# Kernel optimization log

Hardware: AMD Instinct MI355X
Metric: run time of the kernel (lower is better)

## Reference

```python
import jax, jax.numpy as jnp
import numpy as np

CHUNK = 256
ROPE_BASE = 10000.0
EPS = 1e-6


def setup_inputs() -> dict:
    key = jax.random.key(0)
    ks = jax.random.split(key, 8)
    B, N, D, H, K = 4, 8192, 1024, 16, 4
    x = jax.random.normal(ks[0], (B, N, D), dtype=jnp.float32)
    norm_scale = jnp.ones((D,), dtype=jnp.float32)
    conv_w = jax.random.normal(ks[1], (D, 1, K), dtype=jnp.float32) * 0.2
    conv_b = jax.random.normal(ks[2], (D,), dtype=jnp.float32) * 0.02
    in_proj_w = jax.random.normal(ks[3], (D, 3 * D), dtype=jnp.float32) * 0.02
    dt_bias = jax.random.normal(ks[4], (D,), dtype=jnp.float32) * 0.5
    head_mix = jnp.eye(H, dtype=jnp.float32) + 0.02 * jax.random.normal(ks[5], (H, H), dtype=jnp.float32)
    out_proj_w = jax.random.normal(ks[6], (D, D), dtype=jnp.float32) * 0.02
    return {"x": x, "norm_scale": norm_scale, "conv_w": conv_w, "conv_b": conv_b,
            "in_proj_w": in_proj_w, "dt_bias": dt_bias, "head_mix": head_mix,
            "out_proj_w": out_proj_w}


def _rmsnorm(x, scale):
    xf = x.astype(jnp.float32)
    rms = jax.lax.rsqrt(jnp.mean(xf * xf, axis=-1, keepdims=True) + EPS)
    out = scale.astype(jnp.float32) * (xf * rms)
    return jnp.clip(out, -60000.0, 60000.0).astype(x.dtype)


def _rope(v, N, d_head, dtype):
    # v: (B, N, H, d_head); cos/sin: (N, d_head//2)
    half = d_head // 2
    inv_freq = 1.0 / (ROPE_BASE ** (jnp.arange(0, d_head, 2, dtype=jnp.float32) / d_head))
    freqs = jnp.arange(N, dtype=jnp.float32)[:, None] * inv_freq[None, :]
    cos = jnp.cos(freqs).astype(dtype)[None, :, None, :]
    sin = jnp.sin(freqs).astype(dtype)[None, :, None, :]
    v1, v2 = v[..., :half], v[..., half:]
    return jnp.concatenate([v1 * cos - v2 * sin, v1 * sin + v2 * cos], axis=-1)


def reference(x, norm_scale, conv_w, conv_b, in_proj_w, dt_bias, head_mix, out_proj_w):
    residual = x
    B, N, D = x.shape
    H = head_mix.shape[0]
    d_head = D // H
    xn = _rmsnorm(x, norm_scale)

    # depthwise causal conv: torch pads K-1 both sides then truncates to N -> left-pad only
    K = conv_w.shape[-1]
    xc = jax.lax.conv_general_dilated(
        xn.transpose(0, 2, 1), conv_w, window_strides=(1,), padding=[(K - 1, 0)],
        feature_group_count=D, dimension_numbers=("NCH", "OIH", "NCH"))
    xc = (xc + conv_b[None, :, None]).transpose(0, 2, 1)  # (B, N, D)
    xc = xc * jax.nn.sigmoid(xc)  # SiLU

    fused = xc @ in_proj_w  # (B, N, 3D)
    dt_raw, v, gate_raw = jnp.split(fused, 3, axis=-1)
    dt = jnp.clip(jax.nn.softplus(dt_raw.astype(jnp.float32) + dt_bias.astype(jnp.float32)),
                  0.001, 2.0).astype(dt_raw.dtype)
    gate = jax.nn.sigmoid(gate_raw)
    log_alpha = -dt.astype(jnp.float32)

    v_rot = _rope(v.reshape(B, N, H, d_head), N, d_head, x.dtype).reshape(B, N, D)
    v_in = (v_rot * dt).astype(jnp.float32)

    # pad to multiple of CHUNK (static)
    pad = (-N) % CHUNK
    if pad:
        v_in = jnp.pad(v_in, ((0, 0), (0, pad), (0, 0)))
        log_alpha = jnp.pad(log_alpha, ((0, 0), (0, pad), (0, 0)))
    Np = N + pad
    nc = Np // CHUNK
    v_ch = v_in.reshape(B, nc, CHUNK, D)
    la_ch = log_alpha.reshape(B, nc, CHUNK, D)

    # intra-chunk stabilized cumulative scan
    L = jnp.clip(jnp.cumsum(la_ch, axis=2), -20.0, 0.0)
    L_max = jnp.max(L, axis=2, keepdims=True)
    L_st = L - L_max
    cum_scaled = jnp.cumsum(jnp.exp(-L_st) * v_ch, axis=2)
    chunk_out = jnp.exp(L_st) * cum_scaled  # (B, nc, CHUNK, D)

    if nc > 1:
        # inter-chunk carry, fully parallel
        bdecay = L[:, :, -1, :]            # (B, nc, D)
        bout = chunk_out[:, :, -1, :]      # (B, nc, D)
        cum_decay = jnp.clip(jnp.cumsum(bdecay, axis=1), -80.0, 0.0)
        stab = jnp.max(cum_decay, axis=1, keepdims=True)
        ncd = jnp.clip(cum_decay - stab, -20.0, 0.0)
        seeds = bout * jnp.exp(-ncd)
        shifted = jnp.pad(seeds[:, :-1], ((0, 0), (1, 0), (0, 0)))
        carries = jnp.cumsum(shifted, axis=1) * jnp.exp(ncd)  # (B, nc, D)
        final = chunk_out + carries[:, :, None, :] * jnp.exp(L)
    else:
        final = chunk_out
    final = final.astype(x.dtype).reshape(B, Np, D)[:, :N, :]

    v_mix = jnp.einsum("bnhd,hm->bnmd", final.reshape(B, N, H, d_head), head_mix)
    final = v_mix.reshape(B, N, D)
    out = (final * gate) @ out_proj_w
    return residual + out
```

## Files before the change

### kernel.cpp

```cpp
#include <hip/hip_runtime.h>

#define TOK 32768
#define DMODEL 1024
#define NSEQ 8192
#define NCHK 32
#define CHUNKC 256
#define KDIM 1024
#define NKT (KDIM / 32)
#define LOG2E 1.44269504f

typedef __attribute__((ext_vector_type(8))) short bf16x8;
typedef __attribute__((ext_vector_type(4))) float f32x4;

__device__ __forceinline__ unsigned short f2bf(float f) {
  unsigned u = __float_as_uint(f);
  u += 0x7fffu + ((u >> 16) & 1u);
  return (unsigned short)(u >> 16);
}
__device__ __forceinline__ float bf2f(unsigned short h) {
  return __uint_as_float(((unsigned)h) << 16);
}
__device__ __forceinline__ float sigm(float x) {
  return __builtin_amdgcn_rcpf(1.f + exp2f(-LOG2E * x));
}

typedef __attribute__((address_space(3))) unsigned int lds_u32_t;
typedef const __attribute__((address_space(1))) unsigned int glb_u32_t;

__device__ __forceinline__ void gl_lds16(const void* g, void* l) {
  __builtin_amdgcn_global_load_lds((glb_u32_t*)g, (lds_u32_t*)l, 16, 0, 0);
}

__global__ __launch_bounds__(256) void transpose_bf16_k(const float* __restrict__ in,
                                                        unsigned short* __restrict__ out,
                                                        int R, int C) {
  __shared__ float tile[32][33];
  const int c0 = blockIdx.x * 32, r0 = blockIdx.y * 32;
  const int tx = threadIdx.x, ty = threadIdx.y;
#pragma unroll
  for (int i = 0; i < 32; i += 8)
    tile[ty + i][tx] = in[(long)(r0 + ty + i) * C + c0 + tx];
  __syncthreads();
#pragma unroll
  for (int i = 0; i < 32; i += 8)
    out[(long)(c0 + ty + i) * R + r0 + tx] = f2bf(tile[tx][ty + i]);
}

__global__ __launch_bounds__(256) void ropetab_k(float2* __restrict__ tab) {
  const int i = blockIdx.x * 256 + threadIdx.x;
  const int f = i & 31, n = i >> 5;
  const float invf = exp2f(-(float)f * (13.287712379549449f / 32.0f));
  const float ang = (float)n * invf;
  tab[i] = make_float2(cosf(ang), sinf(ang));
}

__global__ __launch_bounds__(256) void rmsconv_k(const float* __restrict__ x,
                                                 const float* __restrict__ scale,
                                                 const float* __restrict__ w,
                                                 const float* __restrict__ cb,
                                                 unsigned short* __restrict__ xc) {
  __shared__ float xs[11][1024];
  __shared__ float red[4];
  const int t = threadIdx.x;
  const long row0 = (long)blockIdx.x * 8;
  const bool seqstart = ((row0 & (NSEQ - 1)) == 0);
  const float4 sc = ((const float4*)scale)[t];
  for (int i = 0; i < 11; ++i) {
    if (i < 3 && seqstart) {
      ((float4*)xs[i])[t] = make_float4(0.f, 0.f, 0.f, 0.f);
      continue;
    }
    const long r = row0 - 3 + i;
    const float4 v = ((const float4*)(x + r * DMODEL))[t];
    float ss = v.x * v.x + v.y * v.y + v.z * v.z + v.w * v.w;
#pragma unroll
    for (int off = 32; off > 0; off >>= 1) ss += __shfl_down(ss, off);
    if ((t & 63) == 0) red[t >> 6] = ss;
    __syncthreads();
    const float tot = red[0] + red[1] + red[2] + red[3];
    const float rr = rsqrtf(tot * (1.0f / DMODEL) + 1e-6f);
    float4 o;
    o.x = fminf(fmaxf(v.x * rr * sc.x, -60000.f), 60000.f);
    o.y = fminf(fmaxf(v.y * rr * sc.y, -60000.f), 60000.f);
    o.z = fminf(fmaxf(v.z * rr * sc.z, -60000.f), 60000.f);
    o.w = fminf(fmaxf(v.w * rr * sc.w, -60000.f), 60000.f);
    ((float4*)xs[i])[t] = o;
    __syncthreads();
  }
  __syncthreads();
  const int d0 = t * 4;
  float wl[4][4];
#pragma unroll
  for (int j = 0; j < 4; ++j) {
    const float4 t4 = *(const float4*)(w + (d0 + j) * 4);
    wl[j][0] = t4.x; wl[j][1] = t4.y; wl[j][2] = t4.z; wl[j][3] = t4.w;
  }
  const float4 cb4 = ((const float4*)cb)[t];
#pragma unroll
  for (int orow = 0; orow < 8; ++orow) {
    float o[4] = {0.f, 0.f, 0.f, 0.f};
#pragma unroll
    for (int k = 0; k < 4; ++k) {
      const float4 xv = ((const float4*)xs[orow + k])[t];
      o[0] += xv.x * wl[0][k]; o[1] += xv.y * wl[1][k];
      o[2] += xv.z * wl[2][k]; o[3] += xv.w * wl[3][k];
    }
    ushort4 st;
    { const float a = o[0] + cb4.x; st.x = f2bf(a * sigm(a)); }
    { const float a = o[1] + cb4.y; st.y = f2bf(a * sigm(a)); }
    { const float a = o[2] + cb4.z; st.z = f2bf(a * sigm(a)); }
    { const float a = o[3] + cb4.w; st.w = f2bf(a * sigm(a)); }
    *(ushort4*)(xc + (row0 + orow) * DMODEL + d0) = st;
  }
}

template <int EPI, int NBN, int SBN>
__global__ __launch_bounds__(256) void gemm_bt(const unsigned short* __restrict__ A,
                                               const unsigned short* __restrict__ BT,
                                               unsigned short* __restrict__ ob,
                                               float* __restrict__ of,
                                               const float* __restrict__ resid) {
  __shared__ unsigned short As[3][128 * 32];
  __shared__ unsigned short Bs[3][256 * 32];
  const int tid = threadIdx.x;
  const int l = tid & 63;
  const int w = tid >> 6;
  constexpr int NC = (EPI == 0) ? 3072 : 1024;

  constexpr int BPS = 4 * SBN;
  constexpr int NBNS = NBN / SBN;
  const int lin = blockIdx.y * NBN + blockIdx.x;
  const int xcd = lin & 7;
  const int g = lin >> 3;
  const int s = g / BPS;
  const int r = g - s * BPS;
  const int bmo = r / SBN;
  const int bno = r - bmo * SBN;
  const int bmS = s / NBNS;
  const int bnS = s - bmS * NBNS;
  const int bm = xcd * 32 + bmS * 4 + bmo;
  const int bn = bnS * SBN + bno;

  f32x4 acc[8][4];
#pragma unroll
  for (int m = 0; m < 8; ++m)
#pragma unroll
    for (int n = 0; n < 4; ++n) acc[m][n] = {0.f, 0.f, 0.f, 0.f};

  const int srcc = (((l & 3) ^ ((l >> 3) & 3)) * 8);
  const unsigned short* aG0 = A + ((long)(bm * 128 + w * 32 + (l >> 2))) * KDIM + srcc;
  const unsigned short* bG0 = BT + ((long)(bn * 256 + w * 64 + (l >> 2))) * KDIM + srcc;
  const int aLo = (w * 32) * 32;
  const int bLo = (w * 64) * 32;

#define STAGE(buf, k0)                                           \
  {                                                              \
    gl_lds16(aG0 + (k0),             &As[buf][aLo]);             \
    gl_lds16(aG0 + (k0) + 16 * KDIM, &As[buf][aLo + 512]);       \
    gl_lds16(bG0 + (k0),             &Bs[buf][bLo]);             \
    gl_lds16(bG0 + (k0) + 16 * KDIM, &Bs[buf][bLo + 512]);       \
    gl_lds16(bG0 + (k0) + 32 * KDIM, &Bs[buf][bLo + 1024]);      \
    gl_lds16(bG0 + (k0) + 48 * KDIM, &Bs[buf][bLo + 1536]);      \
  }

  const int eoff = (((l >> 4) ^ ((l >> 1) & 3)) * 8);
  const int arow0 = (l & 15) * 32 + eoff;
  const int brow0 = (w * 64 + (l & 15)) * 32 + eoff;

  auto compute = [&](int cur) {
    const unsigned short* Ab = &As[cur][0];
    const unsigned short* Bb = &Bs[cur][0];
    bf16x8 af[8], bfr[4];
#pragma unroll
    for (int m = 0; m < 8; ++m) af[m] = *(const bf16x8*)&Ab[arow0 + m * 512];
#pragma unroll
    for (int n = 0; n < 4; ++n) bfr[n] = *(const bf16x8*)&Bb[brow0 + n * 512];
    __builtin_amdgcn_s_setprio(1);
#pragma unroll
    for (int m = 0; m < 8; ++m)
#pragma unroll
      for (int n = 0; n < 4; ++n)
        acc[m][n] = __builtin_amdgcn_mfma_f32_16x16x32_bf16(af[m], bfr[n], acc[m][n], 0, 0, 0);
    __builtin_amdgcn_s_setprio(0);
  };

  STAGE(0, 0);
  STAGE(1, 32);
  asm volatile("s_waitcnt vmcnt(6)" ::: "memory");
  int cur = 0, nxt = 2;
  for (int t = 0; t < NKT - 2; ++t) {
    __builtin_amdgcn_s_barrier();
    __builtin_amdgcn_sched_barrier(0);
    STAGE(nxt, (t + 2) * 32);
    compute(cur);
    asm volatile("s_waitcnt vmcnt(6)" ::: "memory");
    cur = (cur == 2) ? 0 : cur + 1;
    nxt = (nxt == 2) ? 0 : nxt + 1;
  }
  __builtin_amdgcn_s_barrier();
  __builtin_amdgcn_sched_barrier(0);
  compute(cur);
  asm volatile("s_waitcnt vmcnt(0)" ::: "memory");
  cur = (cur == 2) ? 0 : cur + 1;
  __builtin_amdgcn_s_barrier();
  __builtin_amdgcn_sched_barrier(0);
  compute(cur);
#undef STAGE

  const int rbase = bm * 128;
  const int cbase = bn * 256 + w * 64;
  const int lr4 = (l >> 4) * 4;
  const int lc16 = l & 15;

  if constexpr (EPI == 0) {
#pragma unroll
    for (int m = 0; m < 8; ++m)
#pragma unroll
      for (int n = 0; n < 4; ++n) {
        const int col = cbase + n * 16 + lc16;
#pragma unroll
        for (int j2 = 0; j2 < 4; ++j2) {
          const int row = rbase + m * 16 + lr4 + j2;
          ob[(long)row * NC + col] = f2bf(acc[m][n][j2]);
        }
      }
  } else {
#pragma unroll
    for (int m = 0; m < 8; ++m)
#pragma unroll
      for (int n = 0; n < 4; ++n) {
        const int col = cbase + n * 16 + lc16;
#pragma unroll
        for (int j2 = 0; j2 < 4; ++j2) {
          const int row = rbase + m * 16 + lr4 + j2;
          const long o = (long)row * NC + col;
          of[o] = resid[o] + acc[m][n][j2];
        }
      }
  }
}

__global__ __launch_bounds__(256) void scan1_k(const unsigned short* __restrict__ fu,
                                               const float* __restrict__ dt_bias,
                                               const float2* __restrict__ tab,
                                               float* __restrict__ Llast,
                                               float* __restrict__ bout) {
  const int idx = blockIdx.x * 256 + threadIdx.x;
  const int d = idx & 1023;
  const int ch = (idx >> 10) & 31;
  const int b = idx >> 15;
  const long base = ((long)b * NSEQ + ch * CHUNKC) * 3072 + d;
  const float bias = dt_bias[d];
  const int f = d & 31;
  const bool hi = (d & 32) != 0;
  const int po = hi ? -32 : 32;
  float run = 0.f, s = 0.f, L = 0.f;
#pragma unroll 4
  for (int c = 0; c < CHUNKC; ++c) {
    const long o = base + (long)c * 3072;
    const float a = bf2f(fu[o]) + bias;
    const float e2 = exp2f(-LOG2E * fabsf(a));
    const float sp = fmaxf(a, 0.f) + 0.69314718f * log2f(1.f + e2);
    const float dtv = fminf(fmaxf(sp, 0.001f), 2.0f);
    const float own = bf2f(fu[o + 1024]);
    const float oth = bf2f(fu[o + 1024 + po]);
    const float2 cs = tab[(ch * CHUNKC + c) * 32 + f];
    const float vr = own * cs.x + (hi ? oth * cs.y : -oth * cs.y);
    run -= dtv;
    L = fminf(fmaxf(run, -20.f), 0.f);
    s += exp2f(-LOG2E * L) * (vr * dtv);
  }
  Llast[idx] = L;
  bout[idx] = exp2f(LOG2E * L) * s;
}

__global__ __launch_bounds__(256) void scan2_k(const float* __restrict__ Llast,
                                               const float* __restrict__ bout,
                                               float* __restrict__ carry) {
  const int idx = blockIdx.x * 256 + threadIdx.x;
  const int d = idx & 1023;
  const int b = idx >> 10;
  const long base = (long)b * (NCHK * DMODEL) + d;
  float cd[NCHK];
  float run = 0.f, stab = -1e30f;
#pragma unroll
  for (int ch = 0; ch < NCHK; ++ch) {
    run += Llast[base + ch * DMODEL];
    cd[ch] = fminf(fmaxf(run, -80.f), 0.f);
    stab = fmaxf(stab, cd[ch]);
  }
  float acc = 0.f;
#pragma unroll
  for (int ch = 0; ch < NCHK; ++ch) {
    const float ncd = fminf(fmaxf(cd[ch] - stab, -20.f), 0.f);
    carry[base + ch * DMODEL] = acc * exp2f(LOG2E * ncd);
    acc += bout[base + ch * DMODEL] * exp2f(-LOG2E * ncd);
  }
}

__global__ __launch_bounds__(256) void scan3_k(unsigned short* fu,
                                               const float* __restrict__ dt_bias,
                                               const float2* __restrict__ tab,
                                               const float* __restrict__ carry) {
  const int idx = blockIdx.x * 256 + threadIdx.x;
  const int d = idx & 1023;
  const int ch = (idx >> 10) & 31;
  const int b = idx >> 15;
  const long base = ((long)b * NSEQ + ch * CHUNKC) * 3072 + d;
  const float bias = dt_bias[d];
  const int f = d & 31;
  const bool hi = (d & 32) != 0;
  const int po = hi ? -32 : 32;
  const float ce = carry[idx];
  float run = 0.f, s = 0.f;
#pragma unroll 4
  for (int c = 0; c < CHUNKC; ++c) {
    const long o = base + (long)c * 3072;
    const float a = bf2f(fu[o]) + bias;
    const float e2 = exp2f(-LOG2E * fabsf(a));
    const float sp = fmaxf(a, 0.f) + 0.69314718f * log2f(1.f + e2);
    const float dtv = fminf(fmaxf(sp, 0.001f), 2.0f);
    const float own = bf2f(fu[o + 1024]);
    const float oth = bf2f(fu[o + 1024 + po]);
    const float2 cs = tab[(ch * CHUNKC + c) * 32 + f];
    const float vr = own * cs.x + (hi ? oth * cs.y : -oth * cs.y);
    run -= dtv;
    const float L = fminf(fmaxf(run, -20.f), 0.f);
    s += exp2f(-LOG2E * L) * (vr * dtv);
    fu[o + 1024] = f2bf(exp2f(LOG2E * L) * (s + ce));
  }
}

__global__ __launch_bounds__(256) void headmix_k(const unsigned short* __restrict__ fu,
                                                 const float* __restrict__ hm,
                                                 unsigned short* __restrict__ A2) {
  __shared__ float mixs[256];
  const int t = threadIdx.x;
  mixs[t] = hm[t];
  __syncthreads();
  const long row = (long)blockIdx.x * 4 + (t >> 6);
  const int dd = t & 63;
  const unsigned short* fv0 = fu + row * 3072 + 1024 + dd;
  const unsigned short* gv0 = fu + row * 3072 + 2048 + dd;
  float fv[16];
#pragma unroll
  for (int h = 0; h < 16; ++h) fv[h] = bf2f(fv0[h * 64]);
#pragma unroll
  for (int m = 0; m < 16; ++m) {
    float o = 0.f;
#pragma unroll
    for (int h = 0; h < 16; ++h) o += fv[h] * mixs[h * 16 + m];
    A2[row * DMODEL + m * 64 + dd] = f2bf(o * sigm(bf2f(gv0[m * 64])));
  }
}

extern "C" void kernel_launch(void* const* d_in, const int* in_sizes, int n_in,
                              void* d_out, int out_size, void* d_ws, size_t ws_size,
                              hipStream_t stream) {
  const float* x        = (const float*)d_in[0];
  const float* nscale   = (const float*)d_in[1];
  const float* conv_w   = (const float*)d_in[2];
  const float* conv_b   = (const float*)d_in[3];
  const float* in_proj  = (const float*)d_in[4];
  const float* dt_bias  = (const float*)d_in[5];
  const float* head_mix = (const float*)d_in[6];
  const float* out_proj = (const float*)d_in[7];
  float* out = (float*)d_out;

  char* p = (char*)d_ws;
  unsigned short* W1T = (unsigned short*)p; p += (size_t)3072 * 1024 * 2;
  unsigned short* W2T = (unsigned short*)p; p += (size_t)1024 * 1024 * 2;
  float2* tab  = (float2*)p; p += (size_t)NSEQ * 32 * sizeof(float2);
  float* Llast = (float*)p;  p += (size_t)131072 * 4;
  float* bout  = (float*)p;  p += (size_t)131072 * 4;
  float* carry = (float*)p;  p += (size_t)131072 * 4;
  unsigned short* fusedb = (unsigned short*)p; p += (size_t)TOK * 3072 * 2;
  unsigned short* xc     = (unsigned short*)p; p += (size_t)TOK * DMODEL * 2;

  transpose_bf16_k<<<dim3(96, 32), dim3(32, 8), 0, stream>>>(in_proj, W1T, 1024, 3072);
  transpose_bf16_k<<<dim3(32, 32), dim3(32, 8), 0, stream>>>(out_proj, W2T, 1024, 1024);
  ropetab_k<<<1024, 256, 0, stream>>>(tab);
  rmsconv_k<<<TOK / 8, 256, 0, stream>>>(x, nscale, conv_w, conv_b, xc);

  gemm_bt<0, 12, 6><<<dim3(12, 256), 256, 0, stream>>>(xc, W1T, fusedb, nullptr, nullptr);
  scan1_k<<<512, 256, 0, stream>>>(fusedb, dt_bias, tab, Llast, bout);
  scan2_k<<<16, 256, 0, stream>>>(Llast, bout, carry);
  scan3_k<<<512, 256, 0, stream>>>(fusedb, dt_bias, tab, carry);
  headmix_k<<<TOK / 4, 256, 0, stream>>>(fusedb, head_mix, xc );
  gemm_bt<1, 4, 4><<<dim3(4, 256), 256, 0, stream>>>(xc, W2T, nullptr, out, x);
}
```

Baseline: 626.8 us.

## Restructure bf16 GEMM to 256x256 tiles with 8 waves and phased pipelining

The GEMM kernel moves from 128x256 tiles on 4 waves to 256x256 tiles on 8 waves (512 threads), with each wave computing a 128x64 sub-tile. The K loop becomes a two-buffer, two-substep schedule with 64-wide K steps. Each step is split into half-phases that interleave LDS fragment reads, async global-to-LDS staging and MFMA bursts, separated by barriers and explicit waitcnts. The goal is more data reuse per block and better overlap of loads with MFMA work. The cost is more barriers, larger LDS use (64 KB) and fewer blocks on the grid.

New measurement: 656.0 us. 1.05x slower.

```diff
diff --git a/kernel.cpp b/kernel.cpp
--- a/kernel.cpp
+++ b/kernel.cpp
@@ -6,7 +6,6 @@
 #define NCHK 32
 #define CHUNKC 256
 #define KDIM 1024
-#define NKT (KDIM / 32)
 #define LOG2E 1.44269504f
 
 typedef __attribute__((ext_vector_type(8))) short bf16x8;
@@ -115,16 +114,17 @@
 }
 
 template <int EPI, int NBN, int SBN>
-__global__ __launch_bounds__(256) void gemm_bt(const unsigned short* __restrict__ A,
+__global__ __launch_bounds__(512) void gemm_bt(const unsigned short* __restrict__ A,
                                                const unsigned short* __restrict__ BT,
                                                unsigned short* __restrict__ ob,
                                                float* __restrict__ of,
                                                const float* __restrict__ resid) {
-  __shared__ unsigned short As[3][128 * 32];
-  __shared__ unsigned short Bs[3][256 * 32];
+  __shared__ unsigned short As[2][2][8192];
+  __shared__ unsigned short Bs[2][2][8192];
   const int tid = threadIdx.x;
   const int l = tid & 63;
   const int w = tid >> 6;
+  const int wr = w >> 2, wc = w & 3;
   constexpr int NC = (EPI == 0) ? 3072 : 1024;
 
   constexpr int BPS = 4 * SBN;
@@ -138,7 +138,7 @@
   const int bno = r - bmo * SBN;
   const int bmS = s / NBNS;
   const int bnS = s - bmS * NBNS;
-  const int bm = xcd * 32 + bmS * 4 + bmo;
+  const int bm = xcd * 16 + bmS * 4 + bmo;
   const int bn = bnS * SBN + bno;
 
   f32x4 acc[8][4];
@@ -148,67 +148,84 @@
     for (int n = 0; n < 4; ++n) acc[m][n] = {0.f, 0.f, 0.f, 0.f};
 
   const int srcc = (((l & 3) ^ ((l >> 3) & 3)) * 8);
-  const unsigned short* aG0 = A + ((long)(bm * 128 + w * 32 + (l >> 2))) * KDIM + srcc;
-  const unsigned short* bG0 = BT + ((long)(bn * 256 + w * 64 + (l >> 2))) * KDIM + srcc;
-  const int aLo = (w * 32) * 32;
-  const int bLo = (w * 64) * 32;
-
-#define STAGE(buf, k0)                                           \
-  {                                                              \
-    gl_lds16(aG0 + (k0),             &As[buf][aLo]);             \
-    gl_lds16(aG0 + (k0) + 16 * KDIM, &As[buf][aLo + 512]);       \
-    gl_lds16(bG0 + (k0),             &Bs[buf][bLo]);             \
-    gl_lds16(bG0 + (k0) + 16 * KDIM, &Bs[buf][bLo + 512]);       \
-    gl_lds16(bG0 + (k0) + 32 * KDIM, &Bs[buf][bLo + 1024]);      \
-    gl_lds16(bG0 + (k0) + 48 * KDIM, &Bs[buf][bLo + 1536]);      \
-  }
+  const unsigned short* aG0 = A + ((long)(bm * 256 + w * 32 + (l >> 2))) * KDIM + srcc;
+  const unsigned short* bG0 = BT + ((long)(bn * 256 + w * 32 + (l >> 2))) * KDIM + srcc;
+  const int wL0 = w * 1024;
+
+#define STAGE_A(buf, ks, kofs)                                     \
+  { gl_lds16(aG0 + (kofs),            &As[buf][ks][wL0]);          \
+    gl_lds16(aG0 + (kofs) + 16*KDIM,  &As[buf][ks][wL0 + 512]); }
+#define STAGE_B(buf, ks, kofs)                                     \
+  { gl_lds16(bG0 + (kofs),            &Bs[buf][ks][wL0]);          \
+    gl_lds16(bG0 + (kofs) + 16*KDIM,  &Bs[buf][ks][wL0 + 512]); }
 
   const int eoff = (((l >> 4) ^ ((l >> 1) & 3)) * 8);
-  const int arow0 = (l & 15) * 32 + eoff;
-  const int brow0 = (w * 64 + (l & 15)) * 32 + eoff;
-
-  auto compute = [&](int cur) {
-    const unsigned short* Ab = &As[cur][0];
-    const unsigned short* Bb = &Bs[cur][0];
-    bf16x8 af[8], bfr[4];
-#pragma unroll
-    for (int m = 0; m < 8; ++m) af[m] = *(const bf16x8*)&Ab[arow0 + m * 512];
-#pragma unroll
-    for (int n = 0; n < 4; ++n) bfr[n] = *(const bf16x8*)&Bb[brow0 + n * 512];
-    __builtin_amdgcn_s_setprio(1);
-#pragma unroll
-    for (int m = 0; m < 8; ++m)
-#pragma unroll
-      for (int n = 0; n < 4; ++n)
-        acc[m][n] = __builtin_amdgcn_mfma_f32_16x16x32_bf16(af[m], bfr[n], acc[m][n], 0, 0, 0);
-    __builtin_amdgcn_s_setprio(0);
-  };
-
-  STAGE(0, 0);
-  STAGE(1, 32);
-  asm volatile("s_waitcnt vmcnt(6)" ::: "memory");
-  int cur = 0, nxt = 2;
-  for (int t = 0; t < NKT - 2; ++t) {
-    __builtin_amdgcn_s_barrier();
-    __builtin_amdgcn_sched_barrier(0);
-    STAGE(nxt, (t + 2) * 32);
-    compute(cur);
-    asm volatile("s_waitcnt vmcnt(6)" ::: "memory");
-    cur = (cur == 2) ? 0 : cur + 1;
-    nxt = (nxt == 2) ? 0 : nxt + 1;
-  }
+  const int aRowOff = (wr * 128 + (l & 15)) * 32 + eoff;
+  const int bRowOff = (wc * 64 + (l & 15)) * 32 + eoff;
+
+  bf16x8 bf[4];
+
+#define PHASE(buf, ks, h, stg, vmn)                                            \
+  {                                                                            \
+    bf16x8 af[4];                                                              \
+    _Pragma("unroll")                                                          \
+    for (int m = 0; m < 4; ++m)                                                \
+      af[m] = *(const bf16x8*)&As[buf][ks][aRowOff + (h) * 2048 + m * 512];    \
+    if ((h) == 0) {                                                            \
+      _Pragma("unroll")                                                        \
+      for (int n = 0; n < 4; ++n)                                              \
+        bf[n] = *(const bf16x8*)&Bs[buf][ks][bRowOff + n * 512];               \
+    }                                                                          \
+    stg;                                                                       \
+    __builtin_amdgcn_s_barrier();                                              \
+    asm volatile("s_waitcnt lgkmcnt(0)" ::: "memory");                         \
+    __builtin_amdgcn_sched_barrier(0);                                         \
+    __builtin_amdgcn_s_setprio(1);                                             \
+    _Pragma("unroll")                                                          \
+    for (int m = 0; m < 4; ++m)                                                \
+      _Pragma("unroll")                                                        \
+      for (int n = 0; n < 4; ++n)                                              \
+        acc[(h) * 4 + m][n] = __builtin_amdgcn_mfma_f32_16x16x32_bf16(         \
+            af[m], bf[n], acc[(h) * 4 + m][n], 0, 0, 0);                       \
+    __builtin_amdgcn_s_setprio(0);                                             \
+    asm volatile("s_waitcnt vmcnt(" vmn ")" ::: "memory");                     \
+    __builtin_amdgcn_s_barrier();                                              \
+    __builtin_amdgcn_sched_barrier(0);                                         \
+  }
+
+  STAGE_A(0, 0, 0);
+  STAGE_B(0, 0, 0);
+  STAGE_A(0, 1, 32);
+  STAGE_B(0, 1, 32);
+  STAGE_A(1, 0, 64);
+  STAGE_B(1, 0, 64);
+  asm volatile("s_waitcnt vmcnt(8)" ::: "memory");
   __builtin_amdgcn_s_barrier();
   __builtin_amdgcn_sched_barrier(0);
-  compute(cur);
-  asm volatile("s_waitcnt vmcnt(0)" ::: "memory");
-  cur = (cur == 2) ? 0 : cur + 1;
-  __builtin_amdgcn_s_barrier();
-  __builtin_amdgcn_sched_barrier(0);
-  compute(cur);
-#undef STAGE
-
-  const int rbase = bm * 128;
-  const int cbase = bn * 256 + w * 64;
+
+  for (int t = 0; t < 14; ++t) {
+    const int buf = t & 1, bufn = buf ^ 1;
+    const int k1 = (t + 1) * 64 + 32;
+    const int k2 = (t + 2) * 64;
+    PHASE(buf, 0, 0, STAGE_A(bufn, 1, k1), "8");
+    PHASE(buf, 0, 1, STAGE_B(bufn, 1, k1), "8");
+    PHASE(buf, 1, 0, STAGE_A(buf, 0, k2), "8");
+    PHASE(buf, 1, 1, STAGE_B(buf, 0, k2), "8");
+  }
+  PHASE(0, 0, 0, STAGE_A(1, 1, 15 * 64 + 32), "8");
+  PHASE(0, 0, 1, STAGE_B(1, 1, 15 * 64 + 32), "8");
+  PHASE(0, 1, 0, ((void)0), "8");
+  PHASE(0, 1, 1, ((void)0), "4");
+  PHASE(1, 0, 0, ((void)0), "4");
+  PHASE(1, 0, 1, ((void)0), "0");
+  PHASE(1, 1, 0, ((void)0), "0");
+  PHASE(1, 1, 1, ((void)0), "0");
+#undef PHASE
+#undef STAGE_A
+#undef STAGE_B
+
+  const int rbase = bm * 256 + wr * 128;
+  const int cbase = bn * 256 + wc * 64;
   const int lr4 = (l >> 4) * 4;
   const int lc16 = l & 15;
 
@@ -382,10 +399,10 @@
   ropetab_k<<<1024, 256, 0, stream>>>(tab);
   rmsconv_k<<<TOK / 8, 256, 0, stream>>>(x, nscale, conv_w, conv_b, xc);
 
-  gemm_bt<0, 12, 6><<<dim3(12, 256), 256, 0, stream>>>(xc, W1T, fusedb, nullptr, nullptr);
+  gemm_bt<0, 12, 6><<<dim3(12, 128), 512, 0, stream>>>(xc, W1T, fusedb, nullptr, nullptr);
   scan1_k<<<512, 256, 0, stream>>>(fusedb, dt_bias, tab, Llast, bout);
   scan2_k<<<16, 256, 0, stream>>>(Llast, bout, carry);
   scan3_k<<<512, 256, 0, stream>>>(fusedb, dt_bias, tab, carry);
   headmix_k<<<TOK / 4, 256, 0, stream>>>(fusedb, head_mix, xc );
-  gemm_bt<1, 4, 4><<<dim3(4, 256), 256, 0, stream>>>(xc, W2T, nullptr, out, x);
-}
+  gemm_bt<1, 4, 4><<<dim3(4, 128), 512, 0, stream>>>(xc, W2T, nullptr, out, x);
+}
```

## Use 256x256 eight-wave tiled in-projection GEMM and fuse prep kernels

Applied to the files above, without the earlier changes.

Replaces the in-projection GEMM with a 512-thread kernel that computes 256x256 output tiles. It uses double-buffered LDS staging split into 32-wide K halves, fine-grained barrier phases with s_setprio around the MFMA blocks, and an XOR swizzle. The larger tile halves the number of blocks and is meant to raise operand reuse per LDS load and overlap loads with MFMA issue. It also merges the two weight transposes and the RoPE table into one launch, and keeps the rmsnorm rows in registers instead of LDS so the per-row barriers go away. The risks are higher register pressure from the 11 float4 rows and the larger accumulator tile, plus a tightly hand-scheduled wait pattern.

New measurement: 623.0 us. Within noise of the previous version (-0.6%).

```diff
diff --git a/kernel.cpp b/kernel.cpp
--- a/kernel.cpp
+++ b/kernel.cpp
@@ -6,7 +6,6 @@
 #define NCHK 32
 #define CHUNKC 256
 #define KDIM 1024
-#define NKT (KDIM / 32)
 #define LOG2E 1.44269504f
 
 typedef __attribute__((ext_vector_type(8))) short bf16x8;
@@ -31,27 +30,36 @@
   __builtin_amdgcn_global_load_lds((glb_u32_t*)g, (lds_u32_t*)l, 16, 0, 0);
 }
 
-__global__ __launch_bounds__(256) void transpose_bf16_k(const float* __restrict__ in,
-                                                        unsigned short* __restrict__ out,
-                                                        int R, int C) {
+__global__ __launch_bounds__(256) void prep_k(const float* __restrict__ w1,
+                                              const float* __restrict__ w2,
+                                              unsigned short* __restrict__ w1t,
+                                              unsigned short* __restrict__ w2t,
+                                              float2* __restrict__ tab) {
   __shared__ float tile[32][33];
-  const int c0 = blockIdx.x * 32, r0 = blockIdx.y * 32;
-  const int tx = threadIdx.x, ty = threadIdx.y;
-#pragma unroll
-  for (int i = 0; i < 32; i += 8)
-    tile[ty + i][tx] = in[(long)(r0 + ty + i) * C + c0 + tx];
-  __syncthreads();
-#pragma unroll
-  for (int i = 0; i < 32; i += 8)
-    out[(long)(c0 + ty + i) * R + r0 + tx] = f2bf(tile[tx][ty + i]);
-}
-
-__global__ __launch_bounds__(256) void ropetab_k(float2* __restrict__ tab) {
-  const int i = blockIdx.x * 256 + threadIdx.x;
-  const int f = i & 31, n = i >> 5;
-  const float invf = exp2f(-(float)f * (13.287712379549449f / 32.0f));
-  const float ang = (float)n * invf;
-  tab[i] = make_float2(cosf(ang), sinf(ang));
+  const int bid = blockIdx.x;
+  const int t = threadIdx.x;
+  if (bid < 4096) {
+    const float* in;
+    unsigned short* out;
+    int c0, r0;
+    if (bid < 3072) { in = w1; out = w1t; c0 = (bid % 96) * 32; r0 = (bid / 96) * 32; }
+    else            { in = w2; out = w2t; c0 = ((bid - 3072) & 31) * 32; r0 = ((bid - 3072) >> 5) * 32; }
+    const int C = (bid < 3072) ? 3072 : 1024;
+    const int tx = t & 31, ty = t >> 5;
+#pragma unroll
+    for (int i = 0; i < 32; i += 8)
+      tile[ty + i][tx] = in[(long)(r0 + ty + i) * C + c0 + tx];
+    __syncthreads();
+#pragma unroll
+    for (int i = 0; i < 32; i += 8)
+      out[(long)(c0 + ty + i) * 1024 + r0 + tx] = f2bf(tile[tx][ty + i]);
+  } else {
+    const int i = (bid - 4096) * 256 + t;
+    const int f = i & 31, n = i >> 5;
+    const float invf = exp2f(-(float)f * (13.287712379549449f / 32.0f));
+    const float ang = (float)n * invf;
+    tab[i] = make_float2(cosf(ang), sinf(ang));
+  }
 }
 
 __global__ __launch_bounds__(256) void rmsconv_k(const float* __restrict__ x,
@@ -59,35 +67,34 @@
                                                  const float* __restrict__ w,
                                                  const float* __restrict__ cb,
                                                  unsigned short* __restrict__ xc) {
-  __shared__ float xs[11][1024];
-  __shared__ float red[4];
+  __shared__ float red[11][4];
   const int t = threadIdx.x;
   const long row0 = (long)blockIdx.x * 8;
   const bool seqstart = ((row0 & (NSEQ - 1)) == 0);
   const float4 sc = ((const float4*)scale)[t];
+  float4 vr[11];
+#pragma unroll
   for (int i = 0; i < 11; ++i) {
     if (i < 3 && seqstart) {
-      ((float4*)xs[i])[t] = make_float4(0.f, 0.f, 0.f, 0.f);
-      continue;
+      vr[i] = make_float4(0.f, 0.f, 0.f, 0.f);
+    } else {
+      vr[i] = ((const float4*)(x + (row0 - 3 + i) * DMODEL))[t];
     }
-    const long r = row0 - 3 + i;
-    const float4 v = ((const float4*)(x + r * DMODEL))[t];
-    float ss = v.x * v.x + v.y * v.y + v.z * v.z + v.w * v.w;
+    float ss = vr[i].x * vr[i].x + vr[i].y * vr[i].y + vr[i].z * vr[i].z + vr[i].w * vr[i].w;
 #pragma unroll
     for (int off = 32; off > 0; off >>= 1) ss += __shfl_down(ss, off);
-    if ((t & 63) == 0) red[t >> 6] = ss;
-    __syncthreads();
-    const float tot = red[0] + red[1] + red[2] + red[3];
+    if ((t & 63) == 0) red[i][t >> 6] = ss;
+  }
+  __syncthreads();
+#pragma unroll
+  for (int i = 0; i < 11; ++i) {
+    const float tot = red[i][0] + red[i][1] + red[i][2] + red[i][3];
     const float rr = rsqrtf(tot * (1.0f / DMODEL) + 1e-6f);
-    float4 o;
-    o.x = fminf(fmaxf(v.x * rr * sc.x, -60000.f), 60000.f);
-    o.y = fminf(fmaxf(v.y * rr * sc.y, -60000.f), 60000.f);
-    o.z = fminf(fmaxf(v.z * rr * sc.z, -60000.f), 60000.f);
-    o.w = fminf(fmaxf(v.w * rr * sc.w, -60000.f), 60000.f);
-    ((float4*)xs[i])[t] = o;
-    __syncthreads();
-  }
-  __syncthreads();
+    vr[i].x = fminf(fmaxf(vr[i].x * rr * sc.x, -60000.f), 60000.f);
+    vr[i].y = fminf(fmaxf(vr[i].y * rr * sc.y, -60000.f), 60000.f);
+    vr[i].z = fminf(fmaxf(vr[i].z * rr * sc.z, -60000.f), 60000.f);
+    vr[i].w = fminf(fmaxf(vr[i].w * rr * sc.w, -60000.f), 60000.f);
+  }
   const int d0 = t * 4;
   float wl[4][4];
 #pragma unroll
@@ -101,7 +108,7 @@
     float o[4] = {0.f, 0.f, 0.f, 0.f};
 #pragma unroll
     for (int k = 0; k < 4; ++k) {
-      const float4 xv = ((const float4*)xs[orow + k])[t];
+      const float4 xv = vr[orow + k];
       o[0] += xv.x * wl[0][k]; o[1] += xv.y * wl[1][k];
       o[2] += xv.z * wl[2][k]; o[3] += xv.w * wl[3][k];
     }
@@ -114,10 +121,140 @@
   }
 }
 
-template <int EPI, int NBN, int SBN>
-__global__ __launch_bounds__(256) void gemm_bt(const unsigned short* __restrict__ A,
+template <int NBN, int SBN>
+__global__ __launch_bounds__(512) void gemm8_k(const unsigned short* __restrict__ A,
                                                const unsigned short* __restrict__ BT,
-                                               unsigned short* __restrict__ ob,
+                                               unsigned short* __restrict__ ob) {
+  __shared__ unsigned short As[2][2][8192];
+  __shared__ unsigned short Bs[2][2][8192];
+  const int tid = threadIdx.x;
+  const int l = tid & 63;
+  const int w = tid >> 6;
+  const int wr = w >> 2, wc = w & 3;
+  constexpr int NC = 3072;
+
+  constexpr int BPS = 4 * SBN;
+  constexpr int NBNS = NBN / SBN;
+  const int lin = blockIdx.y * NBN + blockIdx.x;
+  const int xcd = lin & 7;
+  const int g = lin >> 3;
+  const int s = g / BPS;
+  const int r = g - s * BPS;
+  const int bmo = r / SBN;
+  const int bno = r - bmo * SBN;
+  const int bmS = s / NBNS;
+  const int bnS = s - bmS * NBNS;
+  const int bm = xcd * 16 + bmS * 4 + bmo;
+  const int bn = bnS * SBN + bno;
+
+  f32x4 acc[8][4];
+#pragma unroll
+  for (int m = 0; m < 8; ++m)
+#pragma unroll
+    for (int n = 0; n < 4; ++n) acc[m][n] = {0.f, 0.f, 0.f, 0.f};
+
+  const int srcc = (((l & 3) ^ ((l >> 3) & 3)) * 8);
+  const unsigned short* aG0 = A + ((long)(bm * 256 + w * 32 + (l >> 2))) * KDIM + srcc;
+  const unsigned short* bG0 = BT + ((long)(bn * 256 + w * 32 + (l >> 2))) * KDIM + srcc;
+  const int wL0 = w * 1024;
+
+#define STAGE_A(buf, ks, kofs)                                     \
+  { gl_lds16(aG0 + (kofs),            &As[buf][ks][wL0]);          \
+    gl_lds16(aG0 + (kofs) + 16*KDIM,  &As[buf][ks][wL0 + 512]); }
+#define STAGE_B(buf, ks, kofs)                                     \
+  { gl_lds16(bG0 + (kofs),            &Bs[buf][ks][wL0]);          \
+    gl_lds16(bG0 + (kofs) + 16*KDIM,  &Bs[buf][ks][wL0 + 512]); }
+
+  const int eoff = (((l >> 4) ^ ((l >> 1) & 3)) * 8);
+  const int aRowOff = (wr * 128 + (l & 15)) * 32 + eoff;
+  const int bRowOff = (wc * 64 + (l & 15)) * 32 + eoff;
+
+  bf16x8 bf[4];
+
+#define VM8 asm volatile("s_waitcnt vmcnt(8)" ::: "memory")
+#define VM4 asm volatile("s_waitcnt vmcnt(4)" ::: "memory")
+#define VM0 asm volatile("s_waitcnt vmcnt(0)" ::: "memory")
+#define NOW ((void)0)
+
+#define PHASE(buf, ks, h, stg, wt)                                             \
+  {                                                                            \
+    bf16x8 af[4];                                                              \
+    _Pragma("unroll")                                                          \
+    for (int m = 0; m < 4; ++m)                                                \
+      af[m] = *(const bf16x8*)&As[buf][ks][aRowOff + (h) * 2048 + m * 512];    \
+    if ((h) == 0) {                                                            \
+      _Pragma("unroll")                                                        \
+      for (int n = 0; n < 4; ++n)                                              \
+        bf[n] = *(const bf16x8*)&Bs[buf][ks][bRowOff + n * 512];               \
+    }                                                                          \
+    stg;                                                                       \
+    __builtin_amdgcn_s_barrier();                                              \
+    asm volatile("s_waitcnt lgkmcnt(0)" ::: "memory");                         \
+    __builtin_amdgcn_sched_barrier(0);                                         \
+    __builtin_amdgcn_s_setprio(1);                                             \
+    _Pragma("unroll")                                                          \
+    for (int m = 0; m < 4; ++m)                                                \
+      _Pragma("unroll")                                                        \
+      for (int n = 0; n < 4; ++n)                                              \
+        acc[(h) * 4 + m][n] = __builtin_amdgcn_mfma_f32_16x16x32_bf16(         \
+            af[m], bf[n], acc[(h) * 4 + m][n], 0, 0, 0);                       \
+    __builtin_amdgcn_s_setprio(0);                                             \
+    wt;                                                                        \
+    __builtin_amdgcn_s_barrier();                                              \
+    __builtin_amdgcn_sched_barrier(0);                                         \
+  }
+
+  STAGE_A(0, 0, 0);
+  STAGE_B(0, 0, 0);
+  STAGE_A(0, 1, 32);
+  STAGE_B(0, 1, 32);
+  STAGE_A(1, 0, 64);
+  STAGE_B(1, 0, 64);
+  VM8;
+  __builtin_amdgcn_s_barrier();
+  __builtin_amdgcn_sched_barrier(0);
+
+  for (int t = 0; t < 14; ++t) {
+    const int buf = t & 1, bufn = buf ^ 1;
+    const int k1 = (t + 1) * 64 + 32;
+    const int k2 = (t + 2) * 64;
+    PHASE(buf, 0, 0, STAGE_A(bufn, 1, k1), NOW);
+    PHASE(buf, 0, 1, STAGE_B(bufn, 1, k1), VM8);
+    PHASE(buf, 1, 0, STAGE_A(buf, 0, k2), NOW);
+    PHASE(buf, 1, 1, STAGE_B(buf, 0, k2), VM8);
+  }
+  PHASE(0, 0, 0, STAGE_A(1, 1, 992), NOW);
+  PHASE(0, 0, 1, STAGE_B(1, 1, 992), VM8);
+  PHASE(0, 1, 0, NOW, NOW);
+  PHASE(0, 1, 1, NOW, VM4);
+  PHASE(1, 0, 0, NOW, NOW);
+  PHASE(1, 0, 1, NOW, VM0);
+  PHASE(1, 1, 0, NOW, NOW);
+  PHASE(1, 1, 1, NOW, NOW);
+#undef PHASE
+#undef STAGE_A
+#undef STAGE_B
+
+  const int rbase = bm * 256 + wr * 128;
+  const int cbase = bn * 256 + wc * 64;
+  const int lr4 = (l >> 4) * 4;
+  const int lc16 = l & 15;
+#pragma unroll
+  for (int m = 0; m < 8; ++m)
+#pragma unroll
+    for (int n = 0; n < 4; ++n) {
+      const int col = cbase + n * 16 + lc16;
+#pragma unroll
+      for (int j2 = 0; j2 < 4; ++j2) {
+        const int row = rbase + m * 16 + lr4 + j2;
+        ob[(long)row * NC + col] = f2bf(acc[m][n][j2]);
+      }
+    }
+}
+
+template <int NBN, int SBN>
+__global__ __launch_bounds__(256) void gemm2_k(const unsigned short* __restrict__ A,
+                                               const unsigned short* __restrict__ BT,
                                                float* __restrict__ of,
                                                const float* __restrict__ resid) {
   __shared__ unsigned short As[3][128 * 32];
@@ -125,7 +262,8 @@
   const int tid = threadIdx.x;
   const int l = tid & 63;
   const int w = tid >> 6;
-  constexpr int NC = (EPI == 0) ? 3072 : 1024;
+  constexpr int NC = 1024;
+  constexpr int NKT = KDIM / 32;
 
   constexpr int BPS = 4 * SBN;
   constexpr int NBNS = NBN / SBN;
@@ -211,33 +349,18 @@
   const int cbase = bn * 256 + w * 64;
   const int lr4 = (l >> 4) * 4;
   const int lc16 = l & 15;
-
-  if constexpr (EPI == 0) {
-#pragma unroll
-    for (int m = 0; m < 8; ++m)
-#pragma unroll
-      for (int n = 0; n < 4; ++n) {
-        const int col = cbase + n * 16 + lc16;
-#pragma unroll
-        for (int j2 = 0; j2 < 4; ++j2) {
-          const int row = rbase + m * 16 + lr4 + j2;
-          ob[(long)row * NC + col] = f2bf(acc[m][n][j2]);
-        }
+#pragma unroll
+  for (int m = 0; m < 8; ++m)
+#pragma unroll
+    for (int n = 0; n < 4; ++n) {
+      const int col = cbase + n * 16 + lc16;
+#pragma unroll
+      for (int j2 = 0; j2 < 4; ++j2) {
+        const int row = rbase + m * 16 + lr4 + j2;
+        const long o = (long)row * NC + col;
+        of[o] = resid[o] + acc[m][n][j2];
       }
-  } else {
-#pragma unroll
-    for (int m = 0; m < 8; ++m)
-#pragma unroll
-      for (int n = 0; n < 4; ++n) {
-        const int col = cbase + n * 16 + lc16;
-#pragma unroll
-        for (int j2 = 0; j2 < 4; ++j2) {
-          const int row = rbase + m * 16 + lr4 + j2;
-          const long o = (long)row * NC + col;
-          of[o] = resid[o] + acc[m][n][j2];
-        }
-      }
-  }
+    }
 }
 
 __global__ __launch_bounds__(256) void scan1_k(const unsigned short* __restrict__ fu,
@@ -377,15 +500,13 @@
   unsigned short* fusedb = (unsigned short*)p; p += (size_t)TOK * 3072 * 2;
   unsigned short* xc     = (unsigned short*)p; p += (size_t)TOK * DMODEL * 2;
 
-  transpose_bf16_k<<<dim3(96, 32), dim3(32, 8), 0, stream>>>(in_proj, W1T, 1024, 3072);
-  transpose_bf16_k<<<dim3(32, 32), dim3(32, 8), 0, stream>>>(out_proj, W2T, 1024, 1024);
-  ropetab_k<<<1024, 256, 0, stream>>>(tab);
+  prep_k<<<5120, 256, 0, stream>>>(in_proj, out_proj, W1T, W2T, tab);
   rmsconv_k<<<TOK / 8, 256, 0, stream>>>(x, nscale, conv_w, conv_b, xc);
 
-  gemm_bt<0, 12, 6><<<dim3(12, 256), 256, 0, stream>>>(xc, W1T, fusedb, nullptr, nullptr);
+  gemm8_k<12, 6><<<dim3(12, 128), 512, 0, stream>>>(xc, W1T, fusedb);
   scan1_k<<<512, 256, 0, stream>>>(fusedb, dt_bias, tab, Llast, bout);
   scan2_k<<<16, 256, 0, stream>>>(Llast, bout, carry);
   scan3_k<<<512, 256, 0, stream>>>(fusedb, dt_bias, tab, carry);
   headmix_k<<<TOK / 4, 256, 0, stream>>>(fusedb, head_mix, xc );
-  gemm_bt<1, 4, 4><<<dim3(4, 256), 256, 0, stream>>>(xc, W2T, nullptr, out, x);
-}
+  gemm2_k<4, 4><<<dim3(4, 256), 256, 0, stream>>>(xc, W2T, out, x);
+}
```
